# Kernel tuning notes

Hardware: AMD Instinct MI355X
Metric: run time of the kernel (lower is better)

## Reference

```python
import math
import jax, jax.numpy as jnp
import numpy as np

HIDDEN = 2048
N_HEADS = 16
N_KV_HEADS = 4
HEAD_DIM = HIDDEN // N_HEADS  # 128
SEQ = 2048
BATCH = 2
RMS_EPS = 1.1920928955078125e-07  # torch float32 eps (nn.RMSNorm default eps=None)


def setup_inputs() -> dict:
    key = jax.random.key(0)
    ks = jax.random.split(key, 8)
    x = jax.random.normal(ks[0], (BATCH, SEQ, HIDDEN), dtype=jnp.float32)
    # RoPE tables, half-rotation layout: [f0..f_{d/2-1}, f0..f_{d/2-1}]
    inv_freq = 1.0 / (10000.0 ** (jnp.arange(0, HEAD_DIM, 2, dtype=jnp.float32) / HEAD_DIM))
    t = jnp.arange(SEQ, dtype=jnp.float32)
    freqs = jnp.outer(t, inv_freq)                      # [S, D/2]
    emb = jnp.concatenate([freqs, freqs], axis=-1)      # [S, D]
    sin, cos = jnp.sin(emb), jnp.cos(emb)
    s = 0.02
    Wq = jax.random.normal(ks[1], (HIDDEN, HIDDEN), dtype=jnp.float32) * s
    Wk = jax.random.normal(ks[2], (HIDDEN, N_KV_HEADS * HEAD_DIM), dtype=jnp.float32) * s
    Wv = jax.random.normal(ks[3], (HIDDEN, N_KV_HEADS * HEAD_DIM), dtype=jnp.float32) * s
    Wo = jax.random.normal(ks[4], (HIDDEN, HIDDEN), dtype=jnp.float32) * s
    q_norm_w = jnp.ones((HEAD_DIM,), dtype=jnp.float32)
    k_norm_w = jnp.ones((HEAD_DIM,), dtype=jnp.float32)
    return {"x": x, "sin": sin, "cos": cos, "Wq": Wq, "Wk": Wk, "Wv": Wv,
            "Wo": Wo, "q_norm_w": q_norm_w, "k_norm_w": k_norm_w}


def _rms_norm(t, w):
    # RMSNorm over last dim (head_dim) with learned weight
    var = jnp.mean(t * t, axis=-1, keepdims=True)
    return t * jax.lax.rsqrt(var + RMS_EPS) * w


def _apply_rope(t, sin, cos):
    # t: [B, H, S, D]; sin/cos: [S, D] broadcast
    half = t.shape[-1] // 2
    rotated = jnp.concatenate([-t[..., half:], t[..., :half]], axis=-1)
    return cos * t + sin * rotated


def reference(x, sin, cos, Wq, Wk, Wv, Wo, q_norm_w, k_norm_w):
    b, s, _ = x.shape
    rep = N_HEADS // N_KV_HEADS
    # Q: proj -> norm -> transpose -> rope
    q = (x @ Wq).reshape(b, s, N_HEADS, HEAD_DIM)
    q = _rms_norm(q, q_norm_w).transpose(0, 2, 1, 3)           # [B, H, S, D]
    q = _apply_rope(q, sin, cos)
    # K: proj -> repeat kv heads -> norm -> transpose -> rope
    k = (x @ Wk).reshape(b, s, N_KV_HEADS, HEAD_DIM)
    k = jnp.repeat(k, rep, axis=2)                              # [B, S, H, D]
    k = _rms_norm(k, k_norm_w).transpose(0, 2, 1, 3)            # [B, H, S, D]
    k = _apply_rope(k, sin, cos)
    # V: proj -> repeat kv heads -> transpose
    v = (x @ Wv).reshape(b, s, N_KV_HEADS, HEAD_DIM)
    v = jnp.repeat(v, rep, axis=2).transpose(0, 2, 1, 3)        # [B, H, S, D]
    # explicit masked softmax attention (materializes [B,H,S,S])
    scores = jnp.einsum('bhqd,bhkd->bhqk', q, k) / math.sqrt(HEAD_DIM)
    causal = jnp.triu(jnp.ones((s, s), dtype=bool), 1)
    scores = jnp.where(causal, -jnp.inf, scores)
    attn = jax.nn.softmax(scores, axis=-1)
    o = jnp.einsum('bhqk,bhkd->bhqd', attn, v)                  # [B, H, S, D]
    o = o.transpose(0, 2, 1, 3).reshape(b, s, HIDDEN)
    return o @ Wo
```

## Files before the change

kernel.cpp:

```cpp
#include <hip/hip_runtime.h>

typedef __attribute__((ext_vector_type(8))) short bf16x8;
typedef __attribute__((ext_vector_type(4))) float f32x4;

#define HIDDEN 2048
#define NH 16
#define NKV 4
#define HD 128
#define SEQ_N 2048
#define NT 4096
#define QKV_N 3072
#define RMS_EPS 1.1920928955078125e-07f
#define QSCALE 0.08838834764831845f

static __device__ __forceinline__ float b2f(unsigned short u) {
  union { unsigned int i; float f; } v; v.i = ((unsigned int)u) << 16; return v.f;
}
static __device__ __forceinline__ unsigned short f2b(float f) {
  union { float f; unsigned int i; } v; v.f = f;
  unsigned int r = (v.i + 0x7fffu + ((v.i >> 16) & 1u)) >> 16;
  return (unsigned short)r;
}
static __device__ __forceinline__ void gload_lds16(const unsigned short* g, unsigned short* l) {
  __builtin_amdgcn_global_load_lds(
      (const __attribute__((address_space(1))) unsigned int*)g,
      (__attribute__((address_space(3))) unsigned int*)l, 16, 0, 0);
}
static __device__ __forceinline__ void store_c(float* p, float v) { *p = v; }
static __device__ __forceinline__ void store_c(unsigned short* p, float v) { *p = f2b(v); }

template <typename OutT>
__device__ __forceinline__ void gemm_tile(
    const unsigned short* __restrict__ A, int lda,
    const unsigned short* __restrict__ BT, int ldb,
    OutT* __restrict__ C, int ldc,
    int K, int m0, int nloc0, int nout0) {
  __shared__ unsigned short As[4096], Bs[4096];
  const int tid  = threadIdx.x;
  const int wid  = tid >> 6, lane = tid & 63;
  const int g    = lane >> 4, cc = lane & 15;
  const int wr   = wid >> 1,  wc = wid & 1;
  const int r0   = tid >> 2;
  const int cb0  = (tid & 3) * 8;

  f32x4 acc[4][4];
#pragma unroll
  for (int i = 0; i < 4; ++i)
#pragma unroll
    for (int j = 0; j < 4; ++j) acc[i][j] = (f32x4){0.f, 0.f, 0.f, 0.f};

  unsigned short* AsW0 = As + wid * 512;
  unsigned short* AsW1 = As + 2048 + wid * 512;
  unsigned short* BsW0 = Bs + wid * 512;
  unsigned short* BsW1 = Bs + 2048 + wid * 512;
  const unsigned short* Ab0 = A  + (size_t)(m0 + r0)        * lda + cb0;
  const unsigned short* Ab1 = A  + (size_t)(m0 + 64 + r0)   * lda + cb0;
  const unsigned short* Bb0 = BT + (size_t)(nloc0 + r0)     * ldb + cb0;
  const unsigned short* Bb1 = BT + (size_t)(nloc0 + 64 + r0)* ldb + cb0;

  for (int kt = 0; kt < K; kt += 32) {
    gload_lds16(Ab0 + kt, AsW0);
    gload_lds16(Ab1 + kt, AsW1);
    gload_lds16(Bb0 + kt, BsW0);
    gload_lds16(Bb1 + kt, BsW1);
    __syncthreads();
    bf16x8 af[4], bfr[4];
#pragma unroll
    for (int mi = 0; mi < 4; ++mi)
      af[mi] = *(const bf16x8*)(As + ((wr * 64 + mi * 16 + cc) * 32 + g * 8));
#pragma unroll
    for (int ni = 0; ni < 4; ++ni)
      bfr[ni] = *(const bf16x8*)(Bs + ((wc * 64 + ni * 16 + cc) * 32 + g * 8));
#pragma unroll
    for (int mi = 0; mi < 4; ++mi)
#pragma unroll
      for (int ni = 0; ni < 4; ++ni)
        acc[mi][ni] = __builtin_amdgcn_mfma_f32_16x16x32_bf16(af[mi], bfr[ni], acc[mi][ni], 0, 0, 0);
    __syncthreads();
  }
#pragma unroll
  for (int mi = 0; mi < 4; ++mi)
#pragma unroll
    for (int ni = 0; ni < 4; ++ni)
#pragma unroll
      for (int j = 0; j < 4; ++j) {
        int row = m0 + wr * 64 + mi * 16 + g * 4 + j;
        int col = nout0 + wc * 64 + ni * 16 + cc;
        store_c(&C[(size_t)row * ldc + col], acc[mi][ni][j]);
      }
}

__global__ __launch_bounds__(256) void k_gemm_qkv(
    const unsigned short* __restrict__ x,
    const unsigned short* __restrict__ WqT,
    const unsigned short* __restrict__ WkT,
    const unsigned short* __restrict__ WvT,
    unsigned short* __restrict__ Praw) {
  int nb = blockIdx.x % 24, mb = blockIdx.x / 24;
  int n0 = nb * 128;
  const unsigned short* BT; int nloc;
  if (n0 < HIDDEN)            { BT = WqT; nloc = n0; }
  else if (n0 < HIDDEN + 512) { BT = WkT; nloc = n0 - HIDDEN; }
  else                        { BT = WvT; nloc = n0 - (HIDDEN + 512); }
  gemm_tile<unsigned short>(x, HIDDEN, BT, HIDDEN, Praw, QKV_N, HIDDEN, mb * 128, nloc, n0);
}

__global__ __launch_bounds__(256) void k_gemm_o(
    const unsigned short* __restrict__ Oa,
    const unsigned short* __restrict__ WoT,
    float* __restrict__ out) {
  int nb = blockIdx.x % 16, mb = blockIdx.x / 16;
  gemm_tile<float>(Oa, HIDDEN, WoT, HIDDEN, out, HIDDEN, HIDDEN, mb * 128, nb * 128, nb * 128);
}

__global__ __launch_bounds__(256) void k_cvt_f2b(
    const float* __restrict__ src, unsigned short* __restrict__ dst) {
  int i = (blockIdx.x * 256 + threadIdx.x) * 8;
  float4 a = *(const float4*)(src + i);
  float4 b = *(const float4*)(src + i + 4);
  bf16x8 v;
  v[0] = (short)f2b(a.x); v[1] = (short)f2b(a.y); v[2] = (short)f2b(a.z); v[3] = (short)f2b(a.w);
  v[4] = (short)f2b(b.x); v[5] = (short)f2b(b.y); v[6] = (short)f2b(b.z); v[7] = (short)f2b(b.w);
  *(bf16x8*)(dst + i) = v;
}

__global__ __launch_bounds__(256) void k_transpose_f2b(
    const float* __restrict__ src, unsigned short* __restrict__ dst,
    int ld_src, int ld_dst, int tilesC) {
  __shared__ float T[64][68];
  int tr = blockIdx.x / tilesC, tc = blockIdx.x % tilesC;
  int r0 = tr * 64, c0 = tc * 64;
  int tid = threadIdx.x;
#pragma unroll
  for (int it = 0; it < 4; ++it) {
    int u = it * 256 + tid;
    int r = u >> 4, cb = (u & 15) * 4;
    float4 v = *(const float4*)(src + (size_t)(r0 + r) * ld_src + c0 + cb);
    T[r][cb] = v.x; T[r][cb + 1] = v.y; T[r][cb + 2] = v.z; T[r][cb + 3] = v.w;
  }
  __syncthreads();
#pragma unroll
  for (int it = 0; it < 2; ++it) {
    int u = it * 256 + tid;
    int dc = u >> 3, rb = (u & 7) * 8;
    bf16x8 v;
#pragma unroll
    for (int j = 0; j < 8; ++j) v[j] = (short)f2b(T[rb + j][dc]);
    *(bf16x8*)(dst + (size_t)(c0 + dc) * ld_dst + r0 + rb) = v;
  }
}

__global__ __launch_bounds__(256) void k_transpose_bb(
    const unsigned short* __restrict__ src, unsigned short* __restrict__ dst,
    int ld_src, int ld_dst, int tilesC) {
  __shared__ unsigned short T[64][80];
  int tr = blockIdx.x / tilesC, tc = blockIdx.x % tilesC;
  int r0 = tr * 64, c0 = tc * 64;
  int tid = threadIdx.x;
#pragma unroll
  for (int it = 0; it < 2; ++it) {
    int u = it * 256 + tid; int r = u >> 3, cb = (u & 7) * 8;
    bf16x8 v = *(const bf16x8*)(src + (size_t)(r0 + r) * ld_src + c0 + cb);
    *(bf16x8*)(&T[r][cb]) = v;
  }
  __syncthreads();
#pragma unroll
  for (int it = 0; it < 2; ++it) {
    int u = it * 256 + tid; int dc = u >> 3, rb = (u & 7) * 8;
    bf16x8 v;
#pragma unroll
    for (int j = 0; j < 8; ++j) v[j] = (short)T[rb + j][dc];
    *(bf16x8*)(dst + (size_t)(c0 + dc) * ld_dst + r0 + rb) = v;
  }
}

__global__ __launch_bounds__(256) void k_qk_post(
    const unsigned short* __restrict__ Praw,
    const float* __restrict__ sinT,
    const float* __restrict__ cosT,
    const float* __restrict__ qw,
    const float* __restrict__ kw,
    unsigned short* __restrict__ Qbuf,
    unsigned short* __restrict__ Kbuf) {
  int wid = threadIdx.x >> 6, lane = threadIdx.x & 63;
  int rid = blockIdx.x * 4 + wid;
  int t = rid / 20, slot = rid - t * 20;
  int b = t >> 11, s = t & 2047;
  const int isq = (slot < 16);
  int cb = isq ? slot * 128 : HIDDEN + (slot - 16) * 128;
  const unsigned short* src = Praw + (size_t)t * QKV_N + cb;
  float x0 = b2f(src[lane]), x1 = b2f(src[lane + 64]);
  float ssq = x0 * x0 + x1 * x1;
#pragma unroll
  for (int mk = 1; mk < 64; mk <<= 1) ssq += __shfl_xor(ssq, mk, 64);
  float r = rsqrtf(ssq * (1.0f / 128.0f) + RMS_EPS);
  const float* w = isq ? qw : kw;
  float n0 = x0 * r * w[lane];
  float n1 = x1 * r * w[lane + 64];
  float c0 = cosT[s * 128 + lane],      s0 = sinT[s * 128 + lane];
  float c1 = cosT[s * 128 + 64 + lane], s1 = sinT[s * 128 + 64 + lane];
  float o0 = c0 * n0 - s0 * n1;
  float o1 = c1 * n1 + s1 * n0;
  unsigned short* dst;
  if (isq) {
    o0 *= QSCALE; o1 *= QSCALE;
    dst = Qbuf + ((size_t)(b * NH + slot) * SEQ_N + s) * HD;
  } else {
    dst = Kbuf + ((size_t)(b * NKV + (slot - 16)) * SEQ_N + s) * HD;
  }
  dst[lane] = f2b(o0);
  dst[lane + 64] = f2b(o1);
}

__global__ __launch_bounds__(256, 2) void k_attn(
    const unsigned short* __restrict__ Q,
    const unsigned short* __restrict__ K,
    const unsigned short* __restrict__ V,
    unsigned short* __restrict__ O) {
  __shared__ unsigned short Ks[2][64 * 128];
  __shared__ unsigned short Vs[2][128 * 64];
  __shared__ unsigned short Ps[4][32 * 64];
  const int tid = threadIdx.x, wid = tid >> 6, lane = tid & 63;
  const int g = lane >> 4, c = lane & 15;
  const int bid = blockIdx.x;
  const int bh = bid & 31;
  const int b = bh >> 4, h = bh & 15;
  const int qbh = (bid >> 5) & 7;
  const int qb = (bid < 256) ? qbh : (15 - qbh);
  const int q0 = qb * 128;
  const int wq0 = q0 + wid * 32;
  const int kv = h >> 2;
  const int nt = q0 / 64 + 2;

  const unsigned short* Qp = Q + (size_t)(b * NH + h) * SEQ_N * HD;
  const unsigned short* Kp = K + (size_t)(b * NKV + kv) * SEQ_N * HD;
  const unsigned short* Vp = V + (size_t)(kv * HD) * NT + b * SEQ_N;

  const int krow_l = lane >> 4;
  const int kcol_l = (lane & 15) * 8;
  const int vrow_l = lane >> 3;
  const int vcol_l = (lane & 7) * 8;

  bf16x8 qfr[2][4];
#pragma unroll
  for (int qi = 0; qi < 2; ++qi)
#pragma unroll
    for (int ks = 0; ks < 4; ++ks)
      qfr[qi][ks] = *(const bf16x8*)(Qp + (size_t)(wq0 + qi * 16 + c) * HD + ks * 32 + g * 8);

  f32x4 o[2][8];
#pragma unroll
  for (int qi = 0; qi < 2; ++qi)
#pragma unroll
    for (int df = 0; df < 8; ++df) o[qi][df] = (f32x4){0.f, 0.f, 0.f, 0.f};
  float m_i[2][4], l_i[2][4];
#pragma unroll
  for (int qi = 0; qi < 2; ++qi)
#pragma unroll
    for (int i = 0; i < 4; ++i) { m_i[qi][i] = -1e30f; l_i[qi][i] = 0.f; }

#define STAGE(BUF, KBASE)                                                          \
  {                                                                                \
    _Pragma("unroll")                                                              \
    for (int ch = 0; ch < 4; ++ch) {                                               \
      int chunk = wid * 4 + ch;                                                    \
      int rk = chunk * 4 + krow_l;                                                 \
      int ck = kcol_l ^ ((rk & 15) << 3);                                          \
      gload_lds16(Kp + (size_t)((KBASE) + rk) * HD + ck, &Ks[BUF][chunk * 512]);   \
      int rv = chunk * 8 + vrow_l;                                                 \
      int cv = vcol_l ^ ((rv & 7) << 3);                                           \
      gload_lds16(Vp + (size_t)rv * NT + (KBASE) + cv, &Vs[BUF][chunk * 512]);     \
    }                                                                              \
  }

  int buf = 0;
  STAGE(0, 0);
  __syncthreads();

  for (int kt = 0; kt < nt; ++kt) {
    const int kbase = kt * 64;
    if (kt + 1 < nt) STAGE(buf ^ 1, kbase + 64);

    if (kbase <= wq0 + 31) {
      f32x4 s[2][4];
#pragma unroll
      for (int qi = 0; qi < 2; ++qi)
#pragma unroll
        for (int kf = 0; kf < 4; ++kf) s[qi][kf] = (f32x4){0.f, 0.f, 0.f, 0.f};
#pragma unroll
      for (int ks = 0; ks < 4; ++ks) {
        bf16x8 bk[4];
#pragma unroll
        for (int kf = 0; kf < 4; ++kf) {
          int r = kf * 16 + c;
          int e = (ks * 32 + g * 8) ^ ((r & 15) << 3);
          bk[kf] = *(const bf16x8*)(&Ks[buf][r * 128 + e]);
        }
#pragma unroll
        for (int qi = 0; qi < 2; ++qi)
#pragma unroll
          for (int kf = 0; kf < 4; ++kf)
            s[qi][kf] = __builtin_amdgcn_mfma_f32_16x16x32_bf16(qfr[qi][ks], bk[kf], s[qi][kf], 0, 0, 0);
      }
      if (kbase + 63 > wq0) {
#pragma unroll
        for (int qi = 0; qi < 2; ++qi)
#pragma unroll
          for (int kf = 0; kf < 4; ++kf)
#pragma unroll
            for (int i = 0; i < 4; ++i) {
              int q = wq0 + qi * 16 + g * 4 + i;
              int kp = kbase + kf * 16 + c;
              if (kp > q) s[qi][kf][i] = -1e30f;
            }
      }
      float scl[2][4];
#pragma unroll
      for (int qi = 0; qi < 2; ++qi)
#pragma unroll
        for (int i = 0; i < 4; ++i) {
          float rm = fmaxf(fmaxf(s[qi][0][i], s[qi][1][i]), fmaxf(s[qi][2][i], s[qi][3][i]));
          rm = fmaxf(rm, __shfl_xor(rm, 1, 64));
          rm = fmaxf(rm, __shfl_xor(rm, 2, 64));
          rm = fmaxf(rm, __shfl_xor(rm, 4, 64));
          rm = fmaxf(rm, __shfl_xor(rm, 8, 64));
          float mn = fmaxf(m_i[qi][i], rm);
          scl[qi][i] = __expf(m_i[qi][i] - mn);
          m_i[qi][i] = mn;
        }
#pragma unroll
      for (int qi = 0; qi < 2; ++qi) {
        float ps[4] = {0.f, 0.f, 0.f, 0.f};
#pragma unroll
        for (int kf = 0; kf < 4; ++kf)
#pragma unroll
          for (int i = 0; i < 4; ++i) {
            float p = __expf(s[qi][kf][i] - m_i[qi][i]);
            ps[i] += p;
            int r = qi * 16 + g * 4 + i;
            int e = (kf * 16 + c) ^ ((r & 7) << 3);
            Ps[wid][r * 64 + e] = f2b(p);
          }
#pragma unroll
        for (int i = 0; i < 4; ++i) {
          float t = ps[i];
          t += __shfl_xor(t, 1, 64);
          t += __shfl_xor(t, 2, 64);
          t += __shfl_xor(t, 4, 64);
          t += __shfl_xor(t, 8, 64);
          l_i[qi][i] = l_i[qi][i] * scl[qi][i] + t;
        }
      }
#pragma unroll
      for (int qi = 0; qi < 2; ++qi)
#pragma unroll
        for (int df = 0; df < 8; ++df) {
          o[qi][df][0] *= scl[qi][0]; o[qi][df][1] *= scl[qi][1];
          o[qi][df][2] *= scl[qi][2]; o[qi][df][3] *= scl[qi][3];
        }
#pragma unroll
      for (int ksp = 0; ksp < 2; ++ksp) {
        bf16x8 pa[2];
#pragma unroll
        for (int qi = 0; qi < 2; ++qi) {
          int r2 = qi * 16 + c;
          int e = (ksp * 32 + g * 8) ^ ((r2 & 7) << 3);
          pa[qi] = *(const bf16x8*)(&Ps[wid][r2 * 64 + e]);
        }
#pragma unroll
        for (int df = 0; df < 8; ++df) {
          int rv = df * 16 + c;
          int e = (ksp * 32 + g * 8) ^ ((rv & 7) << 3);
          bf16x8 vb = *(const bf16x8*)(&Vs[buf][rv * 64 + e]);
#pragma unroll
          for (int qi = 0; qi < 2; ++qi)
            o[qi][df] = __builtin_amdgcn_mfma_f32_16x16x32_bf16(pa[qi], vb, o[qi][df], 0, 0, 0);
        }
      }
    }
    __syncthreads();
    buf ^= 1;
  }

  unsigned short* Op = O + (size_t)(b * SEQ_N) * HIDDEN + h * HD;
#pragma unroll
  for (int qi = 0; qi < 2; ++qi)
#pragma unroll
    for (int i = 0; i < 4; ++i) {
      float inv = 1.0f / l_i[qi][i];
      int q = wq0 + qi * 16 + g * 4 + i;
#pragma unroll
      for (int df = 0; df < 8; ++df)
        Op[(size_t)q * HIDDEN + df * 16 + c] = f2b(o[qi][df][i] * inv);
    }
#undef STAGE
}

extern "C" void kernel_launch(void* const* d_in, const int* in_sizes, int n_in,
                              void* d_out, int out_size, void* d_ws, size_t ws_size,
                              hipStream_t stream) {
  const float* x    = (const float*)d_in[0];
  const float* sinT = (const float*)d_in[1];
  const float* cosT = (const float*)d_in[2];
  const float* Wq   = (const float*)d_in[3];
  const float* Wk   = (const float*)d_in[4];
  const float* Wv   = (const float*)d_in[5];
  const float* Wo   = (const float*)d_in[6];
  const float* qw   = (const float*)d_in[7];
  const float* kw   = (const float*)d_in[8];
  float* out = (float*)d_out;
  unsigned short* ws = (unsigned short*)d_ws;

  unsigned short* Xb   = ws;
  unsigned short* WqT  = ws + 8388608;
  unsigned short* WkT  = ws + 12582912;
  unsigned short* WvT  = ws + 13631488;
  unsigned short* WoT  = ws + 14680064;
  unsigned short* Praw = ws + 18874368;
  unsigned short* Qbuf = ws + 31457280;
  unsigned short* Kbuf = ws + 39845888;
  unsigned short* Vt   = ws + 41943040;
  unsigned short* Oatt = ws + 44040192;

  dim3 blk(256);
  k_cvt_f2b<<<4096, blk, 0, stream>>>(x, Xb);
  k_transpose_f2b<<<1024, blk, 0, stream>>>(Wq, WqT, 2048, 2048, 32);
  k_transpose_f2b<<<256,  blk, 0, stream>>>(Wk, WkT, 512,  2048, 8);
  k_transpose_f2b<<<256,  blk, 0, stream>>>(Wv, WvT, 512,  2048, 8);
  k_transpose_f2b<<<1024, blk, 0, stream>>>(Wo, WoT, 2048, 2048, 32);
  k_gemm_qkv<<<768, blk, 0, stream>>>(Xb, WqT, WkT, WvT, Praw);
  k_qk_post<<<20480, blk, 0, stream>>>(Praw, sinT, cosT, qw, kw, Qbuf, Kbuf);
  k_transpose_bb<<<512, blk, 0, stream>>>(Praw + 2560, Vt, 3072, 4096, 8);
  k_attn<<<512, blk, 0, stream>>>(Qbuf, Kbuf, Vt, Oatt);
  k_gemm_o<<<512, blk, 0, stream>>>(Oatt, WoT, out);
}
```

Measured before the change: 365.6 us.

## Shrink attention query tiles, vectorize QK post, swizzle GEMM block order

```diff
diff --git a/kernel.cpp b/kernel.cpp
--- a/kernel.cpp
+++ b/kernel.cpp
@@ -1,6 +1,7 @@
 #include <hip/hip_runtime.h>
 
 typedef __attribute__((ext_vector_type(8))) short bf16x8;
+typedef __attribute__((ext_vector_type(4))) short bf16x4;
 typedef __attribute__((ext_vector_type(4))) float f32x4;
 
 #define HIDDEN 2048
@@ -96,7 +97,8 @@
     const unsigned short* __restrict__ WkT,
     const unsigned short* __restrict__ WvT,
     unsigned short* __restrict__ Praw) {
-  int nb = blockIdx.x % 24, mb = blockIdx.x / 24;
+  int wg = (blockIdx.x & 7) * 96 + (blockIdx.x >> 3);
+  int nb = wg % 24, mb = wg / 24;
   int n0 = nb * 128;
   const unsigned short* BT; int nloc;
   if (n0 < HIDDEN)            { BT = WqT; nloc = n0; }
@@ -109,7 +111,8 @@
     const unsigned short* __restrict__ Oa,
     const unsigned short* __restrict__ WoT,
     float* __restrict__ out) {
-  int nb = blockIdx.x % 16, mb = blockIdx.x / 16;
+  int wg = (blockIdx.x & 7) * 64 + (blockIdx.x >> 3);
+  int nb = wg % 16, mb = wg / 16;
   gemm_tile<float>(Oa, HIDDEN, WoT, HIDDEN, out, HIDDEN, HIDDEN, mb * 128, nb * 128, nb * 128);
 }
 
@@ -182,34 +185,49 @@
     const float* __restrict__ kw,
     unsigned short* __restrict__ Qbuf,
     unsigned short* __restrict__ Kbuf) {
-  int wid = threadIdx.x >> 6, lane = threadIdx.x & 63;
-  int rid = blockIdx.x * 4 + wid;
+  int sub = threadIdx.x >> 4;
+  int sl  = threadIdx.x & 15;
+  int rid = blockIdx.x * 16 + sub;
   int t = rid / 20, slot = rid - t * 20;
   int b = t >> 11, s = t & 2047;
   const int isq = (slot < 16);
   int cb = isq ? slot * 128 : HIDDEN + (slot - 16) * 128;
   const unsigned short* src = Praw + (size_t)t * QKV_N + cb;
-  float x0 = b2f(src[lane]), x1 = b2f(src[lane + 64]);
-  float ssq = x0 * x0 + x1 * x1;
-#pragma unroll
-  for (int mk = 1; mk < 64; mk <<= 1) ssq += __shfl_xor(ssq, mk, 64);
+  const int d0 = sl * 4;
+  bf16x4 a0 = *(const bf16x4*)(src + d0);
+  bf16x4 a1 = *(const bf16x4*)(src + 64 + d0);
+  float x0[4], x1[4];
+  float ssq = 0.f;
+#pragma unroll
+  for (int j = 0; j < 4; ++j) {
+    x0[j] = b2f((unsigned short)a0[j]);
+    x1[j] = b2f((unsigned short)a1[j]);
+    ssq += x0[j] * x0[j] + x1[j] * x1[j];
+  }
+#pragma unroll
+  for (int mk = 1; mk < 16; mk <<= 1) ssq += __shfl_xor(ssq, mk, 64);
   float r = rsqrtf(ssq * (1.0f / 128.0f) + RMS_EPS);
   const float* w = isq ? qw : kw;
-  float n0 = x0 * r * w[lane];
-  float n1 = x1 * r * w[lane + 64];
-  float c0 = cosT[s * 128 + lane],      s0 = sinT[s * 128 + lane];
-  float c1 = cosT[s * 128 + 64 + lane], s1 = sinT[s * 128 + 64 + lane];
-  float o0 = c0 * n0 - s0 * n1;
-  float o1 = c1 * n1 + s1 * n0;
-  unsigned short* dst;
-  if (isq) {
-    o0 *= QSCALE; o1 *= QSCALE;
-    dst = Qbuf + ((size_t)(b * NH + slot) * SEQ_N + s) * HD;
-  } else {
-    dst = Kbuf + ((size_t)(b * NKV + (slot - 16)) * SEQ_N + s) * HD;
-  }
-  dst[lane] = f2b(o0);
-  dst[lane + 64] = f2b(o1);
+  f32x4 w0 = *(const f32x4*)(w + d0);
+  f32x4 w1 = *(const f32x4*)(w + 64 + d0);
+  f32x4 cs0 = *(const f32x4*)(cosT + s * 128 + d0);
+  f32x4 cs1 = *(const f32x4*)(cosT + s * 128 + 64 + d0);
+  f32x4 sn0 = *(const f32x4*)(sinT + s * 128 + d0);
+  f32x4 sn1 = *(const f32x4*)(sinT + s * 128 + 64 + d0);
+  unsigned short* dst = isq
+      ? Qbuf + ((size_t)(b * NH + slot) * SEQ_N + s) * HD
+      : Kbuf + ((size_t)(b * NKV + (slot - 16)) * SEQ_N + s) * HD;
+  const float qs = isq ? QSCALE : 1.0f;
+  bf16x4 o0, o1;
+#pragma unroll
+  for (int j = 0; j < 4; ++j) {
+    float n0 = x0[j] * r * w0[j];
+    float n1 = x1[j] * r * w1[j];
+    o0[j] = (short)f2b((cs0[j] * n0 - sn0[j] * n1) * qs);
+    o1[j] = (short)f2b((cs1[j] * n1 + sn1[j] * n0) * qs);
+  }
+  *(bf16x4*)(dst + d0) = o0;
+  *(bf16x4*)(dst + 64 + d0) = o1;
 }
 
 __global__ __launch_bounds__(256, 2) void k_attn(
@@ -219,18 +237,18 @@
     unsigned short* __restrict__ O) {
   __shared__ unsigned short Ks[2][64 * 128];
   __shared__ unsigned short Vs[2][128 * 64];
-  __shared__ unsigned short Ps[4][32 * 64];
+  __shared__ unsigned short Ps[4][16 * 64];
   const int tid = threadIdx.x, wid = tid >> 6, lane = tid & 63;
   const int g = lane >> 4, c = lane & 15;
   const int bid = blockIdx.x;
   const int bh = bid & 31;
   const int b = bh >> 4, h = bh & 15;
-  const int qbh = (bid >> 5) & 7;
-  const int qb = (bid < 256) ? qbh : (15 - qbh);
-  const int q0 = qb * 128;
-  const int wq0 = q0 + wid * 32;
+  const int z = bid >> 5;
+  const int zz = z & 7, zr = z >> 3;
+  const int qt = (zr == 0) ? zz : (zr == 1) ? 15 - zz : (zr == 2) ? 16 + zz : 31 - zz;
+  const int wq0 = qt * 64 + wid * 16;
   const int kv = h >> 2;
-  const int nt = q0 / 64 + 2;
+  const int nt = qt + 1;
 
   const unsigned short* Qp = Q + (size_t)(b * NH + h) * SEQ_N * HD;
   const unsigned short* Kp = K + (size_t)(b * NKV + kv) * SEQ_N * HD;
@@ -241,23 +259,16 @@
   const int vrow_l = lane >> 3;
   const int vcol_l = (lane & 7) * 8;
 
-  bf16x8 qfr[2][4];
-#pragma unroll
-  for (int qi = 0; qi < 2; ++qi)
-#pragma unroll
-    for (int ks = 0; ks < 4; ++ks)
-      qfr[qi][ks] = *(const bf16x8*)(Qp + (size_t)(wq0 + qi * 16 + c) * HD + ks * 32 + g * 8);
-
-  f32x4 o[2][8];
-#pragma unroll
-  for (int qi = 0; qi < 2; ++qi)
-#pragma unroll
-    for (int df = 0; df < 8; ++df) o[qi][df] = (f32x4){0.f, 0.f, 0.f, 0.f};
-  float m_i[2][4], l_i[2][4];
-#pragma unroll
-  for (int qi = 0; qi < 2; ++qi)
-#pragma unroll
-    for (int i = 0; i < 4; ++i) { m_i[qi][i] = -1e30f; l_i[qi][i] = 0.f; }
+  bf16x8 qfr[4];
+#pragma unroll
+  for (int ks = 0; ks < 4; ++ks)
+    qfr[ks] = *(const bf16x8*)(Qp + (size_t)(wq0 + c) * HD + ks * 32 + g * 8);
+
+  f32x4 o[8];
+#pragma unroll
+  for (int df = 0; df < 8; ++df) o[df] = (f32x4){0.f, 0.f, 0.f, 0.f};
+  float m_i[4] = {-1e30f, -1e30f, -1e30f, -1e30f};
+  float l_i[4] = {0.f, 0.f, 0.f, 0.f};
 
 #define STAGE(BUF, KBASE)                                                          \
   {                                                                                \
@@ -281,118 +292,98 @@
     const int kbase = kt * 64;
     if (kt + 1 < nt) STAGE(buf ^ 1, kbase + 64);
 
-    if (kbase <= wq0 + 31) {
-      f32x4 s[2][4];
-#pragma unroll
-      for (int qi = 0; qi < 2; ++qi)
-#pragma unroll
-        for (int kf = 0; kf < 4; ++kf) s[qi][kf] = (f32x4){0.f, 0.f, 0.f, 0.f};
-#pragma unroll
-      for (int ks = 0; ks < 4; ++ks) {
-        bf16x8 bk[4];
-#pragma unroll
-        for (int kf = 0; kf < 4; ++kf) {
-          int r = kf * 16 + c;
-          int e = (ks * 32 + g * 8) ^ ((r & 15) << 3);
-          bk[kf] = *(const bf16x8*)(&Ks[buf][r * 128 + e]);
+    f32x4 s[4];
+#pragma unroll
+    for (int kf = 0; kf < 4; ++kf) s[kf] = (f32x4){0.f, 0.f, 0.f, 0.f};
+    __builtin_amdgcn_s_setprio(1);
+#pragma unroll
+    for (int ks = 0; ks < 4; ++ks) {
+      bf16x8 bk[4];
+#pragma unroll
+      for (int kf = 0; kf < 4; ++kf) {
+        int r = kf * 16 + c;
+        int e = (ks * 32 + g * 8) ^ ((r & 15) << 3);
+        bk[kf] = *(const bf16x8*)(&Ks[buf][r * 128 + e]);
+      }
+#pragma unroll
+      for (int kf = 0; kf < 4; ++kf)
+        s[kf] = __builtin_amdgcn_mfma_f32_16x16x32_bf16(qfr[ks], bk[kf], s[kf], 0, 0, 0);
+    }
+    __builtin_amdgcn_s_setprio(0);
+    if (kbase + 63 > wq0) {
+#pragma unroll
+      for (int kf = 0; kf < 4; ++kf)
+#pragma unroll
+        for (int i = 0; i < 4; ++i) {
+          int q = wq0 + g * 4 + i;
+          int kp = kbase + kf * 16 + c;
+          if (kp > q) s[kf][i] = -1e30f;
         }
-#pragma unroll
-        for (int qi = 0; qi < 2; ++qi)
-#pragma unroll
-          for (int kf = 0; kf < 4; ++kf)
-            s[qi][kf] = __builtin_amdgcn_mfma_f32_16x16x32_bf16(qfr[qi][ks], bk[kf], s[qi][kf], 0, 0, 0);
+    }
+    float scl[4];
+#pragma unroll
+    for (int i = 0; i < 4; ++i) {
+      float rm = fmaxf(fmaxf(s[0][i], s[1][i]), fmaxf(s[2][i], s[3][i]));
+      rm = fmaxf(rm, __shfl_xor(rm, 1, 64));
+      rm = fmaxf(rm, __shfl_xor(rm, 2, 64));
+      rm = fmaxf(rm, __shfl_xor(rm, 4, 64));
+      rm = fmaxf(rm, __shfl_xor(rm, 8, 64));
+      float mn = fmaxf(m_i[i], rm);
+      scl[i] = __expf(m_i[i] - mn);
+      m_i[i] = mn;
+    }
+    float ps[4] = {0.f, 0.f, 0.f, 0.f};
+#pragma unroll
+    for (int kf = 0; kf < 4; ++kf)
+#pragma unroll
+      for (int i = 0; i < 4; ++i) {
+        float p = __expf(s[kf][i] - m_i[i]);
+        ps[i] += p;
+        int r = g * 4 + i;
+        int e = (kf * 16 + c) ^ ((r & 7) << 3);
+        Ps[wid][r * 64 + e] = f2b(p);
       }
-      if (kbase + 63 > wq0) {
-#pragma unroll
-        for (int qi = 0; qi < 2; ++qi)
-#pragma unroll
-          for (int kf = 0; kf < 4; ++kf)
-#pragma unroll
-            for (int i = 0; i < 4; ++i) {
-              int q = wq0 + qi * 16 + g * 4 + i;
-              int kp = kbase + kf * 16 + c;
-              if (kp > q) s[qi][kf][i] = -1e30f;
-            }
+#pragma unroll
+    for (int i = 0; i < 4; ++i) {
+      float t = ps[i];
+      t += __shfl_xor(t, 1, 64);
+      t += __shfl_xor(t, 2, 64);
+      t += __shfl_xor(t, 4, 64);
+      t += __shfl_xor(t, 8, 64);
+      l_i[i] = l_i[i] * scl[i] + t;
+    }
+#pragma unroll
+    for (int df = 0; df < 8; ++df) {
+      o[df][0] *= scl[0]; o[df][1] *= scl[1];
+      o[df][2] *= scl[2]; o[df][3] *= scl[3];
+    }
+    __builtin_amdgcn_s_setprio(1);
+#pragma unroll
+    for (int ksp = 0; ksp < 2; ++ksp) {
+      int ep = (ksp * 32 + g * 8) ^ ((c & 7) << 3);
+      bf16x8 pa = *(const bf16x8*)(&Ps[wid][c * 64 + ep]);
+#pragma unroll
+      for (int df = 0; df < 8; ++df) {
+        int rv = df * 16 + c;
+        int e = (ksp * 32 + g * 8) ^ ((rv & 7) << 3);
+        bf16x8 vb = *(const bf16x8*)(&Vs[buf][rv * 64 + e]);
+        o[df] = __builtin_amdgcn_mfma_f32_16x16x32_bf16(pa, vb, o[df], 0, 0, 0);
       }
-      float scl[2][4];
-#pragma unroll
-      for (int qi = 0; qi < 2; ++qi)
-#pragma unroll
-        for (int i = 0; i < 4; ++i) {
-          float rm = fmaxf(fmaxf(s[qi][0][i], s[qi][1][i]), fmaxf(s[qi][2][i], s[qi][3][i]));
-          rm = fmaxf(rm, __shfl_xor(rm, 1, 64));
-          rm = fmaxf(rm, __shfl_xor(rm, 2, 64));
-          rm = fmaxf(rm, __shfl_xor(rm, 4, 64));
-          rm = fmaxf(rm, __shfl_xor(rm, 8, 64));
-          float mn = fmaxf(m_i[qi][i], rm);
-          scl[qi][i] = __expf(m_i[qi][i] - mn);
-          m_i[qi][i] = mn;
-        }
-#pragma unroll
-      for (int qi = 0; qi < 2; ++qi) {
-        float ps[4] = {0.f, 0.f, 0.f, 0.f};
-#pragma unroll
-        for (int kf = 0; kf < 4; ++kf)
-#pragma unroll
-          for (int i = 0; i < 4; ++i) {
-            float p = __expf(s[qi][kf][i] - m_i[qi][i]);
-            ps[i] += p;
-            int r = qi * 16 + g * 4 + i;
-            int e = (kf * 16 + c) ^ ((r & 7) << 3);
-            Ps[wid][r * 64 + e] = f2b(p);
-          }
-#pragma unroll
-        for (int i = 0; i < 4; ++i) {
-          float t = ps[i];
-          t += __shfl_xor(t, 1, 64);
-          t += __shfl_xor(t, 2, 64);
-          t += __shfl_xor(t, 4, 64);
-          t += __shfl_xor(t, 8, 64);
-          l_i[qi][i] = l_i[qi][i] * scl[qi][i] + t;
-        }
-      }
-#pragma unroll
-      for (int qi = 0; qi < 2; ++qi)
-#pragma unroll
-        for (int df = 0; df < 8; ++df) {
-          o[qi][df][0] *= scl[qi][0]; o[qi][df][1] *= scl[qi][1];
-          o[qi][df][2] *= scl[qi][2]; o[qi][df][3] *= scl[qi][3];
-        }
-#pragma unroll
-      for (int ksp = 0; ksp < 2; ++ksp) {
-        bf16x8 pa[2];
-#pragma unroll
-        for (int qi = 0; qi < 2; ++qi) {
-          int r2 = qi * 16 + c;
-          int e = (ksp * 32 + g * 8) ^ ((r2 & 7) << 3);
-          pa[qi] = *(const bf16x8*)(&Ps[wid][r2 * 64 + e]);
-        }
-#pragma unroll
-        for (int df = 0; df < 8; ++df) {
-          int rv = df * 16 + c;
-          int e = (ksp * 32 + g * 8) ^ ((rv & 7) << 3);
-          bf16x8 vb = *(const bf16x8*)(&Vs[buf][rv * 64 + e]);
-#pragma unroll
-          for (int qi = 0; qi < 2; ++qi)
-            o[qi][df] = __builtin_amdgcn_mfma_f32_16x16x32_bf16(pa[qi], vb, o[qi][df], 0, 0, 0);
-        }
-      }
-    }
+    }
+    __builtin_amdgcn_s_setprio(0);
     __syncthreads();
     buf ^= 1;
   }
 
   unsigned short* Op = O + (size_t)(b * SEQ_N) * HIDDEN + h * HD;
 #pragma unroll
-  for (int qi = 0; qi < 2; ++qi)
-#pragma unroll
-    for (int i = 0; i < 4; ++i) {
-      float inv = 1.0f / l_i[qi][i];
-      int q = wq0 + qi * 16 + g * 4 + i;
-#pragma unroll
-      for (int df = 0; df < 8; ++df)
-        Op[(size_t)q * HIDDEN + df * 16 + c] = f2b(o[qi][df][i] * inv);
-    }
+  for (int i = 0; i < 4; ++i) {
+    float inv = 1.0f / l_i[i];
+    int q = wq0 + g * 4 + i;
+#pragma unroll
+    for (int df = 0; df < 8; ++df)
+      Op[(size_t)q * HIDDEN + df * 16 + c] = f2b(o[df][i] * inv);
+  }
 #undef STAGE
 }
 
@@ -429,8 +420,8 @@
   k_transpose_f2b<<<256,  blk, 0, stream>>>(Wv, WvT, 512,  2048, 8);
   k_transpose_f2b<<<1024, blk, 0, stream>>>(Wo, WoT, 2048, 2048, 32);
   k_gemm_qkv<<<768, blk, 0, stream>>>(Xb, WqT, WkT, WvT, Praw);
-  k_qk_post<<<20480, blk, 0, stream>>>(Praw, sinT, cosT, qw, kw, Qbuf, Kbuf);
+  k_qk_post<<<5120, blk, 0, stream>>>(Praw, sinT, cosT, qw, kw, Qbuf, Kbuf);
   k_transpose_bb<<<512, blk, 0, stream>>>(Praw + 2560, Vt, 3072, 4096, 8);
-  k_attn<<<512, blk, 0, stream>>>(Qbuf, Kbuf, Vt, Oatt);
+  k_attn<<<1024, blk, 0, stream>>>(Qbuf, Kbuf, Vt, Oatt);
   k_gemm_o<<<512, blk, 0, stream>>>(Oatt, WoT, out);
 }
```

Result: faster. 350.8 us (-4.1%).
